# Kernel optimization log

Measured on AMD Instinct MI355X. Metric: run time of the kernel, lower is better.

Reference implementation:

```python
import jax, jax.numpy as jnp
import numpy as np

STOCH, DETER, HIDDEN, A, EMBED = 30, 200, 200, 6, 1024
T, B = 64, 512
MIN_STD = 0.1
LN_EPS = 1e-3


def _ln(x, s, b):
    m = jnp.mean(x, -1, keepdims=True)
    v = jnp.mean((x - m) ** 2, -1, keepdims=True)
    return (x - m) * jax.lax.rsqrt(v + LN_EPS) * s + b


def _stats(x):
    mean, std = jnp.split(x, 2, -1)
    return mean, jax.nn.softplus(std) + MIN_STD


def setup_inputs() -> dict:
    key = jax.random.key(0)
    ks = jax.random.split(key, 12)
    w = lambda k, shape, s=0.05: jax.random.normal(k, shape, jnp.float32) * s
    return dict(
        embed=w(ks[0], (T, B, EMBED), 1.0),
        action=w(ks[1], (T, B, A), 1.0),
        is_first=jax.random.randint(ks[2], (T, B), 0, 2).astype(jnp.float32),
        noise_prior=w(ks[3], (T, B, STOCH), 1.0),
        noise_post=w(ks[4], (T, B, STOCH), 1.0),
        w_inp=w(ks[5], (STOCH + A, HIDDEN)),
        ln_inp_s=jnp.ones((HIDDEN,)), ln_inp_b=jnp.zeros((HIDDEN,)),
        w_gru=w(ks[6], (HIDDEN + DETER, 3 * DETER)),
        w_imgout=w(ks[7], (DETER, HIDDEN)),
        ln_img_s=jnp.ones((HIDDEN,)), ln_img_b=jnp.zeros((HIDDEN,)),
        w_obsout=w(ks[8], (DETER + EMBED, HIDDEN)),
        ln_obs_s=jnp.ones((HIDDEN,)), ln_obs_b=jnp.zeros((HIDDEN,)),
        w_ims=w(ks[9], (HIDDEN, 2 * STOCH)), b_ims=jnp.zeros((2 * STOCH,)),
        w_obs=w(ks[10], (HIDDEN, 2 * STOCH)), b_obs=jnp.zeros((2 * STOCH,)),
        w_init=w(ks[11], (1, DETER), 0.1),
    )


def reference(embed, action, is_first, noise_prior, noise_post,
              w_inp, ln_inp_s, ln_inp_b, w_gru, w_imgout, ln_img_s, ln_img_b,
              w_obsout, ln_obs_s, ln_obs_b, w_ims, b_ims, w_obs, b_obs, w_init):
    # learned initial state: deter0 = tanh(W), stoch0 = mode (mean) of img stats
    deter0 = jnp.tanh(w_init) * jnp.ones((B, 1), embed.dtype)          # [B, DETER]
    h0 = jax.nn.silu(_ln(deter0 @ w_imgout, ln_img_s, ln_img_b))
    stoch0, _ = _stats(h0 @ w_ims + b_ims)                              # [B, STOCH]

    def step(carry, xs):
        stoch, deter = carry
        a_t, e_t, f_t, nzp, nzq = xs
        # action magnitude clip with stop-gradient scale
        a = a_t * jax.lax.stop_gradient(1.0 / jnp.maximum(jnp.abs(a_t), 1.0))
        f = f_t[:, None]
        a = a * (1.0 - f)
        stoch = stoch * (1.0 - f) + stoch0 * f
        deter = deter * (1.0 - f) + deter0 * f
        # img_step (prior): inp layers -> GRU cell -> img_out -> stats
        x = jax.nn.silu(_ln(jnp.concatenate([stoch, a], -1) @ w_inp, ln_inp_s, ln_inp_b))
        parts = jnp.concatenate([x, deter], -1) @ w_gru                 # [B, 3*DETER]
        r, c, u = jnp.split(parts, 3, -1)
        r = jax.nn.sigmoid(r)
        c = jnp.tanh(r * c)
        u = jax.nn.sigmoid(u - 1.0)                                     # update_bias = -1
        deter = u * c + (1.0 - u) * deter
        hp = jax.nn.silu(_ln(deter @ w_imgout, ln_img_s, ln_img_b))
        pm, ps = _stats(hp @ w_ims + b_ims)
        prior_stoch = pm + ps * nzp                                     # rsample
        # obs_step (posterior, temp_post=True): concat(deter, embed)
        ho = jax.nn.silu(_ln(jnp.concatenate([deter, e_t], -1) @ w_obsout, ln_obs_s, ln_obs_b))
        qm, qs = _stats(ho @ w_obs + b_obs)
        post_stoch = qm + qs * nzq
        out_t = jnp.concatenate([qm, qs, post_stoch, pm, ps, prior_stoch, deter], -1)
        return (post_stoch, deter), out_t

    _, out = jax.lax.scan(step, (stoch0, deter0),
                          (action, embed, is_first, noise_prior, noise_post))
    return out  # [T, B, 6*STOCH + DETER] = post(mean,std,stoch), prior(mean,std,stoch), deter
```

## Files before the change

### kernel.cpp

```cpp
#include <hip/hip_runtime.h>
#include <math.h>

#define T_STEPS 64
#define BATCH   512

typedef short s16x8 __attribute__((ext_vector_type(8)));
typedef float f32x4 __attribute__((ext_vector_type(4)));

#define MFMA(a,b,c) __builtin_amdgcn_mfma_f32_16x16x32_bf16((a),(b),(c),0,0,0)

__device__ __forceinline__ short f2bf(float x){
    union { float f; unsigned u; } v; v.f = x;
    unsigned r = v.u + 0x7FFFu + ((v.u >> 16) & 1u);
    return (short)(r >> 16);
}
__device__ __forceinline__ float bf2f(short s){
    union { unsigned u; float f; } v; v.u = ((unsigned)(unsigned short)s) << 16;
    return v.f;
}
__device__ __forceinline__ float frcp(float x){ return __builtin_amdgcn_rcpf(x); }
__device__ __forceinline__ float fsig(float x){ return frcp(1.f + __expf(-x)); }
__device__ __forceinline__ float ftanh(float x){ return 1.f - 2.f*frcp(1.f + __expf(2.f*x)); }
__device__ __forceinline__ float sp(float x){ return (x>20.f)? x : __logf(1.f + __expf(x)); }

__device__ __forceinline__ void barx(){
    asm volatile("s_waitcnt lgkmcnt(0)" ::: "memory");
    __builtin_amdgcn_s_barrier();
    asm volatile("" ::: "memory");
}

#define FR_GRU   0
#define FR_INP   494
#define FR_OBSD  520
#define FR_OBSE  611
#define FR_OBS   1027
#define FR_IMG   1055
#define FR_IMS   1146
#define FR_TOT   1174

#define WS_STOCH0 1202176
#define WS_DETER0 1202304
#define WS_E      1203200

__global__ void pack_kernel(const float* w_inp, const float* w_gru, const float* w_imgout,
                            const float* w_obsout, const float* w_ims, const float* w_obs,
                            short* pk){
    int f = blockIdx.x, l = threadIdx.x;
    const float* W; int K, N, ld, KT, k0, rel;
    if      (f < FR_INP ){ W=w_gru;    K=400; N=600; ld=600; KT=13; k0=0;   rel=f; }
    else if (f < FR_OBSD){ W=w_inp;    K=36;  N=200; ld=200; KT=2;  k0=0;   rel=f-FR_INP; }
    else if (f < FR_OBSE){ W=w_obsout; K=200; N=200; ld=200; KT=7;  k0=0;   rel=f-FR_OBSD; }
    else if (f < FR_OBS ){ W=w_obsout; K=1024;N=200; ld=200; KT=32; k0=200; rel=f-FR_OBSE; }
    else if (f < FR_IMG ){ W=w_obs;    K=200; N=60;  ld=60;  KT=7;  k0=0;   rel=f-FR_OBS; }
    else if (f < FR_IMS ){ W=w_imgout; K=200; N=200; ld=200; KT=7;  k0=0;   rel=f-FR_IMG; }
    else                 { W=w_ims;    K=200; N=60;  ld=60;  KT=7;  k0=0;   rel=f-FR_IMS; }
    int nt = rel / KT, kt = rel % KT;
    int col = nt*16 + (l & 15);
    int kb  = kt*32 + (l >> 4)*8;
    s16x8 v;
    #pragma unroll
    for (int e = 0; e < 8; e++){
        int k = kb + e;
        float x = (k < K && col < N) ? W[(size_t)(k + k0)*ld + col] : 0.f;
        v[e] = f2bf(x);
    }
    *(((s16x8*)pk) + (size_t)f*64 + l) = v;
}

__global__ void init_kernel(const float* w_init, const float* w_imgout,
                            const float* ln_img_s, const float* ln_img_b,
                            const float* w_ims, const float* b_ims,
                            float* stoch0, float* deter0){
    __shared__ float d0[200], h0[200], redA[64], redB[64], mv[2];
    int t = threadIdx.x;
    if (t < 200) d0[t] = tanhf(w_init[t]);
    __syncthreads();
    if (t < 200){ float a = 0.f; for (int k = 0; k < 200; k++) a += d0[k]*w_imgout[k*200 + t]; h0[t] = a; }
    __syncthreads();
    if (t < 64){ float s = 0.f, s2 = 0.f;
        for (int j = t; j < 200; j += 64){ float v = h0[j]; s += v; s2 += v*v; }
        redA[t] = s; redB[t] = s2; }
    __syncthreads();
    if (t == 0){ float s = 0.f, s2 = 0.f;
        for (int i = 0; i < 64; i++){ s += redA[i]; s2 += redB[i]; }
        float m = s/200.f, var = s2/200.f - m*m;
        mv[0] = m; mv[1] = rsqrtf(var + 1e-3f); }
    __syncthreads();
    if (t < 200){ float v = (h0[t]-mv[0])*mv[1]*ln_img_s[t] + ln_img_b[t];
        h0[t] = v/(1.f+expf(-v)); }
    __syncthreads();
    if (t < 200) deter0[t] = d0[t];
    if (t < 30){ float a = 0.f; for (int j = 0; j < 200; j++) a += h0[j]*w_ims[j*60 + t];
        stoch0[t] = a + b_ims[t]; }
}

__global__ __launch_bounds__(256) void embed_gemm(const float* embed, const short* pk, short* E){
    int tid = threadIdx.x; int w = tid >> 6, l = tid & 63;
    int row0 = blockIdx.x*128 + w*32;
    const float* A0 = embed + (size_t)(row0 + (l & 15))*1024 + (l >> 4)*8;
    const float* A1 = A0 + (size_t)16*1024;
    const s16x8* B = ((const s16x8*)pk) + (size_t)FR_OBSE*64 + l;
    f32x4 acc0[13], acc1[13];
    #pragma unroll
    for (int n = 0; n < 13; n++){ acc0[n] = (f32x4){0.f,0.f,0.f,0.f}; acc1[n] = (f32x4){0.f,0.f,0.f,0.f}; }
    for (int kt = 0; kt < 32; kt++){
        float4 x0 = *(const float4*)(A0 + kt*32), x1 = *(const float4*)(A0 + kt*32 + 4);
        float4 y0 = *(const float4*)(A1 + kt*32), y1 = *(const float4*)(A1 + kt*32 + 4);
        s16x8 af0, af1;
        af0[0]=f2bf(x0.x); af0[1]=f2bf(x0.y); af0[2]=f2bf(x0.z); af0[3]=f2bf(x0.w);
        af0[4]=f2bf(x1.x); af0[5]=f2bf(x1.y); af0[6]=f2bf(x1.z); af0[7]=f2bf(x1.w);
        af1[0]=f2bf(y0.x); af1[1]=f2bf(y0.y); af1[2]=f2bf(y0.z); af1[3]=f2bf(y0.w);
        af1[4]=f2bf(y1.x); af1[5]=f2bf(y1.y); af1[6]=f2bf(y1.z); af1[7]=f2bf(y1.w);
        #pragma unroll
        for (int n = 0; n < 13; n++){
            s16x8 bf = B[(n*32 + kt)*64];
            acc0[n] = MFMA(af0, bf, acc0[n]);
            acc1[n] = MFMA(af1, bf, acc1[n]);
        }
    }
    int rr = (l >> 4)*4, cc = l & 15;
    #pragma unroll
    for (int n = 0; n < 13; n++){
        int col = n*16 + cc;
        if (col < 200){
            #pragma unroll
            for (int r = 0; r < 4; r++){
                E[(size_t)(row0 + rr + r)*200 + col]        = f2bf(acc0[n][r]);
                E[(size_t)(row0 + 16 + rr + r)*200 + col]   = f2bf(acc1[n][r]);
            }
        }
    }
}

#define AB_STRIDE 424
#define XP_STRIDE 210
#define PB_STRIDE 612
#define QP_STRIDE 68
#define A36_STRIDE 72
#define HO_STRIDE 224

__global__ __launch_bounds__(512) void scan_kernel(
    const float* action, const float* is_first, const float* noise_post,
    const float* ln_inp_s, const float* ln_inp_b,
    const float* ln_obs_s, const float* ln_obs_b,
    const float* b_obs,
    const short* pk, const short* E, const float* stoch0g, const float* deter0g,
    float* out)
{
    __shared__ short Abuf[16*AB_STRIDE];
    __shared__ __align__(16) char Uraw[19584];
    __shared__ short A36hob[16*HO_STRIDE];
    __shared__ float Sbuf[16*30];
    __shared__ short WI[26*512];
    __shared__ short WD[91*512];

    float* Uf  = (float*)Uraw;
    short* Pbs = (short*)Uraw;

    int tid = threadIdx.x;
    int w = tid >> 6, l = tid & 63;
    int row = tid >> 5, s = tid & 31;
    int r0 = blockIdx.x*16;
    const int rr = (l >> 4)*4, cc = l & 15;
    const s16x8* PK = (const s16x8*)pk;

    for (int f = w; f < 26; f += 8)
        *(s16x8*)&WI[f*512 + l*8] = PK[(size_t)(FR_INP + f)*64 + l];
    for (int f = w; f < 91; f += 8)
        *(s16x8*)&WD[f*512 + l*8] = PK[(size_t)(FR_OBSD + f)*64 + l];

    float dreg[7];
    #pragma unroll
    for (int i = 0; i < 7; i++){ int j = s + 32*i; dreg[i] = (j < 200) ? deter0g[j] : 0.f; }
    if (s < 30) Sbuf[row*30 + s] = stoch0g[s];
    for (int idx = tid; idx < 16*24; idx += 512){ int q = idx/24; Abuf[q*AB_STRIDE + 400 + idx%24] = 0; }
    #pragma unroll
    for (int i = 0; i < 7; i++){ int j = s + 32*i; if (j < 200) Abuf[row*AB_STRIDE + 200 + j] = f2bf(dreg[i]); }

    float lisr[7], libr[7], losr[7], lobr[7];
    #pragma unroll
    for (int i = 0; i < 7; i++){ int j = s + 32*i; bool ok = j < 200;
        lisr[i] = ok ? ln_inp_s[j] : 0.f;  libr[i] = ok ? ln_inp_b[j] : 0.f;
        losr[i] = ok ? ln_obs_s[j] : 0.f;  lobr[i] = ok ? ln_obs_b[j] : 0.f;
    }
    float bo0 = 0.f, bo1 = 0.f;
    if (tid < 480){ int j = tid % 30; bo0 = b_obs[j]; bo1 = b_obs[30 + j]; }

    barx();

    for (int t = 0; t < T_STEPS; t++){
        float f = is_first[(size_t)t*BATCH + r0 + row];
        #pragma unroll
        for (int i = 0; i < 7; i++){ int j = s + 32*i; if (j < 200){
            float d = dreg[i]*(1.f - f) + deter0g[j]*f;
            dreg[i] = d;
            Abuf[row*AB_STRIDE + 200 + j] = f2bf(d);
        }}
        for (int j = s; j < 64; j += 32){
            float v = 0.f;
            if (j < 30) v = Sbuf[row*30 + j]*(1.f - f) + stoch0g[j]*f;
            else if (j < 36){
                float a = action[(size_t)((size_t)t*BATCH + r0 + row)*6 + (j - 30)];
                a = a * frcp(fmaxf(fabsf(a), 1.f));
                v = a*(1.f - f);
            }
            A36hob[row*A36_STRIDE + j] = f2bf(v);
        }
        s16x8 Ech;
        if (tid < 400){
            int er = tid/25, eq = tid%25;
            Ech = *(((const s16x8*)(E + (size_t)((size_t)t*BATCH + r0 + er)*200)) + eq);
        }
        float nz = 0.f;
        if (tid < 480){
            int rw = tid/30, j = tid%30;
            nz = noise_post[(size_t)((size_t)t*BATCH + r0 + rw)*30 + j];
        }
        barx();

        {
            s16x8 a0 = *(s16x8*)&A36hob[(l & 15)*A36_STRIDE + (l >> 4)*8];
            s16x8 a1 = *(s16x8*)&A36hob[(l & 15)*A36_STRIDE + 32 + (l >> 4)*8];
            for (int nt = w; nt < 13; nt += 8){
                f32x4 acc = (f32x4){0.f,0.f,0.f,0.f};
                acc = MFMA(a0, *(const s16x8*)&WI[(nt*2+0)*512 + l*8], acc);
                acc = MFMA(a1, *(const s16x8*)&WI[(nt*2+1)*512 + l*8], acc);
                #pragma unroll
                for (int r = 0; r < 4; r++) Uf[(rr + r)*XP_STRIDE + nt*16 + cc] = acc[r];
            }
        }
        barx();

        {
            float sum = 0.f, sq = 0.f, vals[7];
            #pragma unroll
            for (int i = 0; i < 7; i++){ int j = s + 32*i;
                float v = (j < 200) ? Uf[row*XP_STRIDE + j] : 0.f;
                vals[i] = v; sum += v; sq += v*v; }
            #pragma unroll
            for (int m = 16; m >= 1; m >>= 1){ sum += __shfl_xor(sum, m); sq += __shfl_xor(sq, m); }
            float mean = sum/200.f, var = sq/200.f - mean*mean, rstd = rsqrtf(var + 1e-3f);
            #pragma unroll
            for (int i = 0; i < 7; i++){ int j = s + 32*i; if (j < 200){
                float v = (vals[i] - mean)*rstd*lisr[i] + libr[i];
                Abuf[row*AB_STRIDE + j] = f2bf(v*fsig(v));
            }}
        }
        barx();

        {
            s16x8 af[13];
            #pragma unroll
            for (int kt = 0; kt < 13; kt++)
                af[kt] = *(s16x8*)&Abuf[(l & 15)*AB_STRIDE + kt*32 + (l >> 4)*8];
            for (int nt = w; nt < 38; nt += 8){
                f32x4 acc = (f32x4){0.f,0.f,0.f,0.f};
                const s16x8* B = PK + (size_t)(FR_GRU + nt*13)*64 + l;
                #pragma unroll
                for (int kt = 0; kt < 13; kt++) acc = MFMA(af[kt], B[kt*64], acc);
                #pragma unroll
                for (int r = 0; r < 4; r++) Pbs[(rr + r)*PB_STRIDE + nt*16 + cc] = f2bf(acc[r]);
            }
        }
        barx();

        {
            float* outp = out + (size_t)((size_t)t*BATCH + r0 + row)*380;
            #pragma unroll
            for (int i = 0; i < 7; i++){ int j = s + 32*i; if (j < 200){
                float rv = bf2f(Pbs[row*PB_STRIDE + j]);
                float cv = bf2f(Pbs[row*PB_STRIDE + 200 + j]);
                float uv = bf2f(Pbs[row*PB_STRIDE + 400 + j]);
                float rg = fsig(rv);
                float cg = ftanh(rg*cv);
                float ug = fsig(uv - 1.f);
                float d  = ug*cg + (1.f - ug)*dreg[i];
                dreg[i] = d;
                Abuf[row*AB_STRIDE + 200 + j] = f2bf(d);
                outp[180 + j] = d;
            }}
        }
        barx();

        {
            s16x8 ad[7];
            #pragma unroll
            for (int kt = 0; kt < 7; kt++)
                ad[kt] = *(s16x8*)&Abuf[(l & 15)*AB_STRIDE + 200 + kt*32 + (l >> 4)*8];
            for (int nt = w; nt < 13; nt += 8){
                f32x4 a0={0.f,0.f,0.f,0.f}, a1={0.f,0.f,0.f,0.f};
                a0 = MFMA(ad[0], *(const s16x8*)&WD[(nt*7+0)*512 + l*8], a0);
                a1 = MFMA(ad[1], *(const s16x8*)&WD[(nt*7+1)*512 + l*8], a1);
                a0 = MFMA(ad[2], *(const s16x8*)&WD[(nt*7+2)*512 + l*8], a0);
                a1 = MFMA(ad[3], *(const s16x8*)&WD[(nt*7+3)*512 + l*8], a1);
                a0 = MFMA(ad[4], *(const s16x8*)&WD[(nt*7+4)*512 + l*8], a0);
                a1 = MFMA(ad[5], *(const s16x8*)&WD[(nt*7+5)*512 + l*8], a1);
                a0 = MFMA(ad[6], *(const s16x8*)&WD[(nt*7+6)*512 + l*8], a0);
                #pragma unroll
                for (int r = 0; r < 4; r++) Uf[(rr + r)*XP_STRIDE + nt*16 + cc] = a0[r]+a1[r];
            }
        }
        barx();

        if (tid < 400){
            int er = tid/25, eq = tid%25;
            #pragma unroll
            for (int e = 0; e < 8; e++) Uf[er*XP_STRIDE + eq*8 + e] += bf2f(Ech[e]);
        }
        barx();

        {
            float sum = 0.f, sq = 0.f, vals[7];
            #pragma unroll
            for (int i = 0; i < 7; i++){ int j = s + 32*i;
                float v = (j < 200) ? Uf[row*XP_STRIDE + j] : 0.f;
                vals[i] = v; sum += v; sq += v*v; }
            #pragma unroll
            for (int m = 16; m >= 1; m >>= 1){ sum += __shfl_xor(sum, m); sq += __shfl_xor(sq, m); }
            float mean = sum/200.f, var = sq/200.f - mean*mean, rstd = rsqrtf(var + 1e-3f);
            #pragma unroll
            for (int i = 0; i < 7; i++){ int j = s + 32*i;
                short hv = 0;
                if (j < 200){
                    float v = (vals[i] - mean)*rstd*losr[i] + lobr[i];
                    hv = f2bf(v*fsig(v));
                }
                A36hob[row*HO_STRIDE + j] = hv;
            }
        }
        barx();

        if (w < 4){
            s16x8 ah[7];
            #pragma unroll
            for (int kt = 0; kt < 7; kt++)
                ah[kt] = *(s16x8*)&A36hob[(l & 15)*HO_STRIDE + kt*32 + (l >> 4)*8];
            f32x4 a0={0.f,0.f,0.f,0.f}, a1={0.f,0.f,0.f,0.f};
            const s16x8* B = PK + (size_t)(FR_OBS + w*7)*64 + l;
            a0=MFMA(ah[0],B[0*64],a0); a1=MFMA(ah[1],B[1*64],a1);
            a0=MFMA(ah[2],B[2*64],a0); a1=MFMA(ah[3],B[3*64],a1);
            a0=MFMA(ah[4],B[4*64],a0); a1=MFMA(ah[5],B[5*64],a1);
            a0=MFMA(ah[6],B[6*64],a0);
            #pragma unroll
            for (int r = 0; r < 4; r++) Uf[(rr + r)*QP_STRIDE + w*16 + cc] = a0[r]+a1[r];
        }
        barx();

        if (tid < 480){
            int rw = tid/30, j = tid%30;
            float qm = Uf[rw*QP_STRIDE + j] + bo0;
            float x  = Uf[rw*QP_STRIDE + 30 + j] + bo1;
            float qs = sp(x) + 0.1f;
            float post = qm + qs*nz;
            float* outp = out + (size_t)((size_t)t*BATCH + r0 + rw)*380;
            outp[j] = qm; outp[30 + j] = qs; outp[60 + j] = post;
            Sbuf[rw*30 + j] = post;
        }
        barx();
    }
}

__global__ __launch_bounds__(64) void prior_kernel(const float* noise_prior, const float* b_ims,
                                                   const float* ln_img_s, const float* ln_img_b,
                                                   const short* pk, float* out){
    __shared__ short Ab[16*232];
    __shared__ float U[16*212];
    __shared__ short hob[16*224];
    __shared__ float qp[16*68];
    int l = threadIdx.x;
    int g0 = blockIdx.x*16;

    for (int idx = l; idx < 16*232; idx += 64){
        int rr = idx/232, c = idx%232;
        short v = 0;
        if (c < 200) v = f2bf(out[(size_t)(g0 + rr)*380 + 180 + c]);
        Ab[idx] = v;
    }
    __syncthreads();
    {
        s16x8 af[7];
        #pragma unroll
        for (int kt = 0; kt < 7; kt++)
            af[kt] = *(s16x8*)&Ab[(l & 15)*232 + kt*32 + (l >> 4)*8];
        for (int nt = 0; nt < 13; nt++){
            f32x4 acc = (f32x4){0.f,0.f,0.f,0.f};
            const s16x8* B = ((const s16x8*)pk) + (size_t)(FR_IMG + nt*7)*64 + l;
            #pragma unroll
            for (int kt = 0; kt < 7; kt++) acc = MFMA(af[kt], B[kt*64], acc);
            int rr = (l >> 4)*4, cc = l & 15;
            #pragma unroll
            for (int r = 0; r < 4; r++) U[(rr + r)*212 + nt*16 + cc] = acc[r];
        }
    }
    __syncthreads();
    {
        int rw = l >> 2, s4 = l & 3;
        float sum = 0.f, sq = 0.f, vals[50];
        #pragma unroll
        for (int i = 0; i < 50; i++){ int j = s4 + 4*i; float v = U[rw*212 + j];
            vals[i] = v; sum += v; sq += v*v; }
        sum += __shfl_xor(sum, 1); sq += __shfl_xor(sq, 1);
        sum += __shfl_xor(sum, 2); sq += __shfl_xor(sq, 2);
        float mean = sum/200.f, var = sq/200.f - mean*mean, rstd = rsqrtf(var + 1e-3f);
        #pragma unroll
        for (int i = 0; i < 50; i++){ int j = s4 + 4*i;
            float v = (vals[i] - mean)*rstd*ln_img_s[j] + ln_img_b[j];
            hob[rw*224 + j] = f2bf(v*fsig(v));
        }
    }
    for (int idx = l; idx < 16*24; idx += 64){ int rr = idx/24; hob[rr*224 + 200 + idx%24] = 0; }
    __syncthreads();
    for (int nt = 0; nt < 4; nt++){
        s16x8 af[7];
        #pragma unroll
        for (int kt = 0; kt < 7; kt++)
            af[kt] = *(s16x8*)&hob[(l & 15)*224 + kt*32 + (l >> 4)*8];
        f32x4 acc = (f32x4){0.f,0.f,0.f,0.f};
        const s16x8* B = ((const s16x8*)pk) + (size_t)(FR_IMS + nt*7)*64 + l;
        #pragma unroll
        for (int kt = 0; kt < 7; kt++) acc = MFMA(af[kt], B[kt*64], acc);
        int rr = (l >> 4)*4, cc = l & 15;
        #pragma unroll
        for (int r = 0; r < 4; r++) qp[(rr + r)*68 + nt*16 + cc] = acc[r];
    }
    __syncthreads();
    for (int idx = l; idx < 480; idx += 64){
        int rw = idx/30, j = idx%30;
        float pm = qp[rw*68 + j] + b_ims[j];
        float x  = qp[rw*68 + 30 + j] + b_ims[30 + j];
        float ps = sp(x) + 0.1f;
        float nz = noise_prior[(size_t)(g0 + rw)*30 + j];
        float prior = pm + ps*nz;
        float* op = out + (size_t)(g0 + rw)*380;
        op[90 + j] = pm; op[120 + j] = ps; op[150 + j] = prior;
    }
}

extern "C" void kernel_launch(void* const* d_in, const int* in_sizes, int n_in,
                              void* d_out, int out_size, void* d_ws, size_t ws_size,
                              hipStream_t stream){
    const float* embed    = (const float*)d_in[0];
    const float* action   = (const float*)d_in[1];
    const float* is_first = (const float*)d_in[2];
    const float* nzp      = (const float*)d_in[3];
    const float* nzq      = (const float*)d_in[4];
    const float* w_inp    = (const float*)d_in[5];
    const float* ln_inp_s = (const float*)d_in[6];
    const float* ln_inp_b = (const float*)d_in[7];
    const float* w_gru    = (const float*)d_in[8];
    const float* w_imgout = (const float*)d_in[9];
    const float* ln_img_s = (const float*)d_in[10];
    const float* ln_img_b = (const float*)d_in[11];
    const float* w_obsout = (const float*)d_in[12];
    const float* ln_obs_s = (const float*)d_in[13];
    const float* ln_obs_b = (const float*)d_in[14];
    const float* w_ims    = (const float*)d_in[15];
    const float* b_ims    = (const float*)d_in[16];
    const float* w_obs    = (const float*)d_in[17];
    const float* b_obs    = (const float*)d_in[18];
    const float* w_init   = (const float*)d_in[19];

    char*  ws    = (char*)d_ws;
    short* pk    = (short*)ws;
    float* stoch0 = (float*)(ws + WS_STOCH0);
    float* deter0 = (float*)(ws + WS_DETER0);
    short* E      = (short*)(ws + WS_E);
    float* out    = (float*)d_out;

    hipLaunchKernelGGL(pack_kernel, dim3(FR_TOT), dim3(64), 0, stream,
                       w_inp, w_gru, w_imgout, w_obsout, w_ims, w_obs, pk);
    hipLaunchKernelGGL(init_kernel, dim3(1), dim3(256), 0, stream,
                       w_init, w_imgout, ln_img_s, ln_img_b, w_ims, b_ims, stoch0, deter0);
    hipLaunchKernelGGL(embed_gemm, dim3(256), dim3(256), 0, stream, embed, pk, E);
    hipLaunchKernelGGL(scan_kernel, dim3(32), dim3(512), 0, stream,
                       action, is_first, nzq, ln_inp_s, ln_inp_b, ln_obs_s, ln_obs_b, b_obs,
                       pk, E, stoch0, deter0, out);
    hipLaunchKernelGGL(prior_kernel, dim3(2048), dim3(64), 0, stream, nzp, b_ims, ln_img_s, ln_img_b, pk, out);
}
```

Before: 888.2 us.

## Split GRU matmul into deter and input halves, overlap deter part with input MLP

The GRU weight is packed as two separate K=200 halves, for the hidden input and for the deter state. Six warps compute the deter-half GRU products while the other two warps run the input projection and its layernorm/SiLU. The x-half is then accumulated on top of the partial results stored as bf16 in shared memory. This moves work off the serial critical path of each step, at the cost of an extra bf16 rounding of the partial sums and an uneven split of work across warps.

```diff
diff --git a/kernel.cpp b/kernel.cpp
--- a/kernel.cpp
+++ b/kernel.cpp
@@ -29,25 +29,27 @@
     asm volatile("" ::: "memory");
 }
 
-#define FR_GRU   0
-#define FR_INP   494
-#define FR_OBSD  520
-#define FR_OBSE  611
-#define FR_OBS   1027
-#define FR_IMG   1055
-#define FR_IMS   1146
-#define FR_TOT   1174
-
-#define WS_STOCH0 1202176
-#define WS_DETER0 1202304
-#define WS_E      1203200
+#define FR_GRUX 0
+#define FR_GRUD 266
+#define FR_INP  532
+#define FR_OBSD 558
+#define FR_OBSE 649
+#define FR_OBS  1065
+#define FR_IMG  1093
+#define FR_IMS  1184
+#define FR_TOT  1212
+
+#define WS_STOCH0 1241088
+#define WS_DETER0 1241216
+#define WS_E      1242112
 
 __global__ void pack_kernel(const float* w_inp, const float* w_gru, const float* w_imgout,
                             const float* w_obsout, const float* w_ims, const float* w_obs,
                             short* pk){
     int f = blockIdx.x, l = threadIdx.x;
     const float* W; int K, N, ld, KT, k0, rel;
-    if      (f < FR_INP ){ W=w_gru;    K=400; N=600; ld=600; KT=13; k0=0;   rel=f; }
+    if      (f < FR_GRUD){ W=w_gru;    K=200; N=600; ld=600; KT=7;  k0=0;   rel=f; }
+    else if (f < FR_INP ){ W=w_gru;    K=200; N=600; ld=600; KT=7;  k0=200; rel=f-FR_GRUD; }
     else if (f < FR_OBSD){ W=w_inp;    K=36;  N=200; ld=200; KT=2;  k0=0;   rel=f-FR_INP; }
     else if (f < FR_OBSE){ W=w_obsout; K=200; N=200; ld=200; KT=7;  k0=0;   rel=f-FR_OBSD; }
     else if (f < FR_OBS ){ W=w_obsout; K=1024;N=200; ld=200; KT=32; k0=200; rel=f-FR_OBSE; }
@@ -139,6 +141,12 @@
 #define A36_STRIDE 72
 #define HO_STRIDE 224
 
+#define MM7(AD, BP, P0, P1) \
+    P0 = MFMA(AD[0], BP[0*64], P0);  P1 = MFMA(AD[1], BP[1*64], P1); \
+    P0 = MFMA(AD[2], BP[2*64], P0);  P1 = MFMA(AD[3], BP[3*64], P1); \
+    P0 = MFMA(AD[4], BP[4*64], P0);  P1 = MFMA(AD[5], BP[5*64], P1); \
+    P0 = MFMA(AD[6], BP[6*64], P0);
+
 __global__ __launch_bounds__(512) void scan_kernel(
     const float* action, const float* is_first, const float* noise_post,
     const float* ln_inp_s, const float* ln_inp_b,
@@ -218,48 +226,88 @@
         }
         barx();
 
-        {
-            s16x8 a0 = *(s16x8*)&A36hob[(l & 15)*A36_STRIDE + (l >> 4)*8];
-            s16x8 a1 = *(s16x8*)&A36hob[(l & 15)*A36_STRIDE + 32 + (l >> 4)*8];
-            for (int nt = w; nt < 13; nt += 8){
+        if (w < 6){
+            s16x8 ad[7];
+            #pragma unroll
+            for (int kt = 0; kt < 7; kt++)
+                ad[kt] = *(s16x8*)&Abuf[cc*AB_STRIDE + 200 + kt*32 + (l>>4)*8];
+            #pragma unroll
+            for (int it = 0; it < 2; it++){
+                int nt = w + it*6;
+                f32x4 p0={0.f,0.f,0.f,0.f}, p1={0.f,0.f,0.f,0.f};
+                const s16x8* B = PK + (size_t)(FR_GRUD + nt*7)*64 + l;
+                MM7(ad, B, p0, p1);
+                #pragma unroll
+                for (int r = 0; r < 4; r++) Pbs[(rr+r)*PB_STRIDE + nt*16 + cc] = f2bf(p0[r]+p1[r]);
+            }
+        } else {
+            s16x8 a0 = *(s16x8*)&A36hob[cc*A36_STRIDE + (l>>4)*8];
+            s16x8 a1 = *(s16x8*)&A36hob[cc*A36_STRIDE + 32 + (l>>4)*8];
+            int nt0 = (w == 6) ? 0 : 7, nt1 = (w == 6) ? 7 : 13;
+            for (int nt = nt0; nt < nt1; nt++){
                 f32x4 acc = (f32x4){0.f,0.f,0.f,0.f};
                 acc = MFMA(a0, *(const s16x8*)&WI[(nt*2+0)*512 + l*8], acc);
                 acc = MFMA(a1, *(const s16x8*)&WI[(nt*2+1)*512 + l*8], acc);
                 #pragma unroll
-                for (int r = 0; r < 4; r++) Uf[(rr + r)*XP_STRIDE + nt*16 + cc] = acc[r];
+                for (int r = 0; r < 4; r++){
+                    int col = nt*16 + cc;
+                    if (col < 200) Abuf[(rr+r)*AB_STRIDE + col] = f2bf(acc[r]);
+                }
+            }
+        }
+        barx();
+
+        if (w < 6){
+            s16x8 ad[7];
+            #pragma unroll
+            for (int kt = 0; kt < 7; kt++)
+                ad[kt] = *(s16x8*)&Abuf[cc*AB_STRIDE + 200 + kt*32 + (l>>4)*8];
+            #pragma unroll
+            for (int it = 2; it < 7; it++){
+                int nt = w + it*6;
+                if (nt < 38){
+                    f32x4 p0={0.f,0.f,0.f,0.f}, p1={0.f,0.f,0.f,0.f};
+                    const s16x8* B = PK + (size_t)(FR_GRUD + nt*7)*64 + l;
+                    MM7(ad, B, p0, p1);
+                    #pragma unroll
+                    for (int r = 0; r < 4; r++) Pbs[(rr+r)*PB_STRIDE + nt*16 + cc] = f2bf(p0[r]+p1[r]);
+                }
+            }
+        } else {
+            int ss = l & 31;
+            #pragma unroll
+            for (int iter = 0; iter < 4; iter++){
+                int row2 = (w-6)*2 + (l>>5) + iter*4;
+                float vals[7], sum = 0.f, sq = 0.f;
+                #pragma unroll
+                for (int i = 0; i < 7; i++){ int j = ss + 32*i;
+                    float v = (j < 200) ? bf2f(Abuf[row2*AB_STRIDE + j]) : 0.f;
+                    vals[i] = v; sum += v; sq += v*v; }
+                #pragma unroll
+                for (int m = 16; m >= 1; m >>= 1){ sum += __shfl_xor(sum, m); sq += __shfl_xor(sq, m); }
+                float mean = sum/200.f, var = sq/200.f - mean*mean, rstd = rsqrtf(var + 1e-3f);
+                #pragma unroll
+                for (int i = 0; i < 7; i++){ int j = ss + 32*i; if (j < 200){
+                    float v = (vals[i] - mean)*rstd*lisr[i] + libr[i];
+                    Abuf[row2*AB_STRIDE + j] = f2bf(v*fsig(v));
+                }}
             }
         }
         barx();
 
         {
-            float sum = 0.f, sq = 0.f, vals[7];
-            #pragma unroll
-            for (int i = 0; i < 7; i++){ int j = s + 32*i;
-                float v = (j < 200) ? Uf[row*XP_STRIDE + j] : 0.f;
-                vals[i] = v; sum += v; sq += v*v; }
-            #pragma unroll
-            for (int m = 16; m >= 1; m >>= 1){ sum += __shfl_xor(sum, m); sq += __shfl_xor(sq, m); }
-            float mean = sum/200.f, var = sq/200.f - mean*mean, rstd = rsqrtf(var + 1e-3f);
-            #pragma unroll
-            for (int i = 0; i < 7; i++){ int j = s + 32*i; if (j < 200){
-                float v = (vals[i] - mean)*rstd*lisr[i] + libr[i];
-                Abuf[row*AB_STRIDE + j] = f2bf(v*fsig(v));
-            }}
-        }
-        barx();
-
-        {
-            s16x8 af[13];
-            #pragma unroll
-            for (int kt = 0; kt < 13; kt++)
-                af[kt] = *(s16x8*)&Abuf[(l & 15)*AB_STRIDE + kt*32 + (l >> 4)*8];
+            s16x8 ax[7];
+            #pragma unroll
+            for (int kt = 0; kt < 7; kt++)
+                ax[kt] = *(s16x8*)&Abuf[cc*AB_STRIDE + kt*32 + (l>>4)*8];
             for (int nt = w; nt < 38; nt += 8){
-                f32x4 acc = (f32x4){0.f,0.f,0.f,0.f};
-                const s16x8* B = PK + (size_t)(FR_GRU + nt*13)*64 + l;
-                #pragma unroll
-                for (int kt = 0; kt < 13; kt++) acc = MFMA(af[kt], B[kt*64], acc);
-                #pragma unroll
-                for (int r = 0; r < 4; r++) Pbs[(rr + r)*PB_STRIDE + nt*16 + cc] = f2bf(acc[r]);
+                f32x4 p0, p1 = (f32x4){0.f,0.f,0.f,0.f};
+                #pragma unroll
+                for (int r = 0; r < 4; r++) p0[r] = bf2f(Pbs[(rr+r)*PB_STRIDE + nt*16 + cc]);
+                const s16x8* B = PK + (size_t)(FR_GRUX + nt*7)*64 + l;
+                MM7(ax, B, p0, p1);
+                #pragma unroll
+                for (int r = 0; r < 4; r++) Pbs[(rr+r)*PB_STRIDE + nt*16 + cc] = f2bf(p0[r]+p1[r]);
             }
         }
         barx();
@@ -286,7 +334,7 @@
             s16x8 ad[7];
             #pragma unroll
             for (int kt = 0; kt < 7; kt++)
-                ad[kt] = *(s16x8*)&Abuf[(l & 15)*AB_STRIDE + 200 + kt*32 + (l >> 4)*8];
+                ad[kt] = *(s16x8*)&Abuf[cc*AB_STRIDE + 200 + kt*32 + (l>>4)*8];
             for (int nt = w; nt < 13; nt += 8){
                 f32x4 a0={0.f,0.f,0.f,0.f}, a1={0.f,0.f,0.f,0.f};
                 a0 = MFMA(ad[0], *(const s16x8*)&WD[(nt*7+0)*512 + l*8], a0);
@@ -334,13 +382,10 @@
             s16x8 ah[7];
             #pragma unroll
             for (int kt = 0; kt < 7; kt++)
-                ah[kt] = *(s16x8*)&A36hob[(l & 15)*HO_STRIDE + kt*32 + (l >> 4)*8];
+                ah[kt] = *(s16x8*)&A36hob[cc*HO_STRIDE + kt*32 + (l>>4)*8];
             f32x4 a0={0.f,0.f,0.f,0.f}, a1={0.f,0.f,0.f,0.f};
             const s16x8* B = PK + (size_t)(FR_OBS + w*7)*64 + l;
-            a0=MFMA(ah[0],B[0*64],a0); a1=MFMA(ah[1],B[1*64],a1);
-            a0=MFMA(ah[2],B[2*64],a0); a1=MFMA(ah[3],B[3*64],a1);
-            a0=MFMA(ah[4],B[4*64],a0); a1=MFMA(ah[5],B[5*64],a1);
-            a0=MFMA(ah[6],B[6*64],a0);
+            MM7(ah, B, a0, a1);
             #pragma unroll
             for (int r = 0; r < 4; r++) Uf[(rr + r)*QP_STRIDE + w*16 + cc] = a0[r]+a1[r];
         }
```

Measured after the change: 922.5 us. +3.9%, slower.

## Stage prior-kernel weights in LDS and process four row tiles per block

Applied to the files above, without the earlier changes.

The prior kernel now runs 256-thread blocks that load the imgout and ims weight fragments into shared memory once, then loop over four 16-row tiles, so weights are read from global memory a quarter as often. Work within each tile is split across four waves, with LayerNorm reduced per 32-lane group and the MFMA chains split into two accumulators. The prior pass is a small part of total time next to the sequential scan, and the larger LDS footprint (about 160KB) limits occupancy to one block per CU.

```diff
diff --git a/kernel.cpp b/kernel.cpp
--- a/kernel.cpp
+++ b/kernel.cpp
@@ -360,79 +360,123 @@
     }
 }
 
-__global__ __launch_bounds__(64) void prior_kernel(const float* noise_prior, const float* b_ims,
-                                                   const float* ln_img_s, const float* ln_img_b,
-                                                   const short* pk, float* out){
-    __shared__ short Ab[16*232];
-    __shared__ float U[16*212];
-    __shared__ short hob[16*224];
-    __shared__ float qp[16*68];
-    int l = threadIdx.x;
-    int g0 = blockIdx.x*16;
-
-    for (int idx = l; idx < 16*232; idx += 64){
-        int rr = idx/232, c = idx%232;
-        short v = 0;
-        if (c < 200) v = f2bf(out[(size_t)(g0 + rr)*380 + 180 + c]);
-        Ab[idx] = v;
-    }
+#define PAB 232
+#define PU  212
+#define PHO 224
+#define PQP 68
+
+__global__ __launch_bounds__(256) void prior_kernel(const float* noise_prior, const float* b_ims,
+                                                    const float* ln_img_s, const float* ln_img_b,
+                                                    const short* pk, float* out){
+    __shared__ short WG[91*512];
+    __shared__ short WS2[28*512];
+    __shared__ short Ab[16*PAB];
+    __shared__ float U[16*PU];
+    __shared__ short hob[16*PHO];
+    __shared__ float qp[16*PQP];
+
+    const int tid = threadIdx.x;
+    const int w = tid >> 6, l = tid & 63;
+    const int rr = (l >> 4)*4, cc = l & 15;
+    const int s = tid & 31;
+    const s16x8* PK = (const s16x8*)pk;
+    const int g0 = blockIdx.x*64;
+
+    for (int f = w; f < 91; f += 4)
+        *(s16x8*)&WG[f*512 + l*8] = PK[(size_t)(FR_IMG + f)*64 + l];
+    for (int f = w; f < 28; f += 4)
+        *(s16x8*)&WS2[f*512 + l*8] = PK[(size_t)(FR_IMS + f)*64 + l];
+
+    float lgs[7], lgb[7];
+    #pragma unroll
+    for (int i = 0; i < 7; i++){ int j = s + 32*i; bool ok = j < 200;
+        lgs[i] = ok ? ln_img_s[j] : 0.f;  lgb[i] = ok ? ln_img_b[j] : 0.f; }
+    float bi0 = b_ims[tid % 30], bi1 = b_ims[30 + tid % 30];
+
+    for (int idx = tid; idx < 16*32; idx += 256) Ab[(idx/32)*PAB + 200 + (idx%32)] = 0;
+    for (int idx = tid; idx < 16*24; idx += 256) hob[(idx/24)*PHO + 200 + (idx%24)] = 0;
+
     __syncthreads();
-    {
-        s16x8 af[7];
+
+    for (int tile = 0; tile < 4; tile++){
+        const int gt = g0 + tile*16;
+
+        for (int idx = tid; idx < 16*200; idx += 256){
+            int q = idx/200, c = idx%200;
+            Ab[q*PAB + c] = f2bf(out[(size_t)(gt + q)*380 + 180 + c]);
+        }
+        barx();
+
+        {
+            s16x8 af[7];
+            #pragma unroll
+            for (int kt = 0; kt < 7; kt++)
+                af[kt] = *(s16x8*)&Ab[(l & 15)*PAB + kt*32 + (l >> 4)*8];
+            for (int nt = w; nt < 13; nt += 4){
+                f32x4 a0={0.f,0.f,0.f,0.f}, a1={0.f,0.f,0.f,0.f};
+                a0 = MFMA(af[0], *(const s16x8*)&WG[(nt*7+0)*512 + l*8], a0);
+                a1 = MFMA(af[1], *(const s16x8*)&WG[(nt*7+1)*512 + l*8], a1);
+                a0 = MFMA(af[2], *(const s16x8*)&WG[(nt*7+2)*512 + l*8], a0);
+                a1 = MFMA(af[3], *(const s16x8*)&WG[(nt*7+3)*512 + l*8], a1);
+                a0 = MFMA(af[4], *(const s16x8*)&WG[(nt*7+4)*512 + l*8], a0);
+                a1 = MFMA(af[5], *(const s16x8*)&WG[(nt*7+5)*512 + l*8], a1);
+                a0 = MFMA(af[6], *(const s16x8*)&WG[(nt*7+6)*512 + l*8], a0);
+                #pragma unroll
+                for (int r = 0; r < 4; r++) U[(rr + r)*PU + nt*16 + cc] = a0[r]+a1[r];
+            }
+        }
+        barx();
+
         #pragma unroll
-        for (int kt = 0; kt < 7; kt++)
-            af[kt] = *(s16x8*)&Ab[(l & 15)*232 + kt*32 + (l >> 4)*8];
-        for (int nt = 0; nt < 13; nt++){
-            f32x4 acc = (f32x4){0.f,0.f,0.f,0.f};
-            const s16x8* B = ((const s16x8*)pk) + (size_t)(FR_IMG + nt*7)*64 + l;
-            #pragma unroll
-            for (int kt = 0; kt < 7; kt++) acc = MFMA(af[kt], B[kt*64], acc);
-            int rr = (l >> 4)*4, cc = l & 15;
-            #pragma unroll
-            for (int r = 0; r < 4; r++) U[(rr + r)*212 + nt*16 + cc] = acc[r];
-        }
-    }
-    __syncthreads();
-    {
-        int rw = l >> 2, s4 = l & 3;
-        float sum = 0.f, sq = 0.f, vals[50];
-        #pragma unroll
-        for (int i = 0; i < 50; i++){ int j = s4 + 4*i; float v = U[rw*212 + j];
-            vals[i] = v; sum += v; sq += v*v; }
-        sum += __shfl_xor(sum, 1); sq += __shfl_xor(sq, 1);
-        sum += __shfl_xor(sum, 2); sq += __shfl_xor(sq, 2);
-        float mean = sum/200.f, var = sq/200.f - mean*mean, rstd = rsqrtf(var + 1e-3f);
-        #pragma unroll
-        for (int i = 0; i < 50; i++){ int j = s4 + 4*i;
-            float v = (vals[i] - mean)*rstd*ln_img_s[j] + ln_img_b[j];
-            hob[rw*224 + j] = f2bf(v*fsig(v));
-        }
-    }
-    for (int idx = l; idx < 16*24; idx += 64){ int rr = idx/24; hob[rr*224 + 200 + idx%24] = 0; }
-    __syncthreads();
-    for (int nt = 0; nt < 4; nt++){
-        s16x8 af[7];
-        #pragma unroll
-        for (int kt = 0; kt < 7; kt++)
-            af[kt] = *(s16x8*)&hob[(l & 15)*224 + kt*32 + (l >> 4)*8];
-        f32x4 acc = (f32x4){0.f,0.f,0.f,0.f};
-        const s16x8* B = ((const s16x8*)pk) + (size_t)(FR_IMS + nt*7)*64 + l;
-        #pragma unroll
-        for (int kt = 0; kt < 7; kt++) acc = MFMA(af[kt], B[kt*64], acc);
-        int rr = (l >> 4)*4, cc = l & 15;
-        #pragma unroll
-        for (int r = 0; r < 4; r++) qp[(rr + r)*68 + nt*16 + cc] = acc[r];
-    }
-    __syncthreads();
-    for (int idx = l; idx < 480; idx += 64){
-        int rw = idx/30, j = idx%30;
-        float pm = qp[rw*68 + j] + b_ims[j];
-        float x  = qp[rw*68 + 30 + j] + b_ims[30 + j];
-        float ps = sp(x) + 0.1f;
-        float nz = noise_prior[(size_t)(g0 + rw)*30 + j];
-        float prior = pm + ps*nz;
-        float* op = out + (size_t)(g0 + rw)*380;
-        op[90 + j] = pm; op[120 + j] = ps; op[150 + j] = prior;
+        for (int iter = 0; iter < 2; iter++){
+            int rw = (tid >> 5) + iter*8;
+            float sum = 0.f, sq = 0.f, vals[7];
+            #pragma unroll
+            for (int i = 0; i < 7; i++){ int j = s + 32*i;
+                float v = (j < 200) ? U[rw*PU + j] : 0.f;
+                vals[i] = v; sum += v; sq += v*v; }
+            #pragma unroll
+            for (int m = 16; m >= 1; m >>= 1){ sum += __shfl_xor(sum, m); sq += __shfl_xor(sq, m); }
+            float mean = sum/200.f, var = sq/200.f - mean*mean, rstd = rsqrtf(var + 1e-3f);
+            #pragma unroll
+            for (int i = 0; i < 7; i++){ int j = s + 32*i; if (j < 200){
+                float v = (vals[i] - mean)*rstd*lgs[i] + lgb[i];
+                hob[rw*PHO + j] = f2bf(v*fsig(v));
+            }}
+        }
+        barx();
+
+        {
+            s16x8 ah[7];
+            #pragma unroll
+            for (int kt = 0; kt < 7; kt++)
+                ah[kt] = *(s16x8*)&hob[(l & 15)*PHO + kt*32 + (l >> 4)*8];
+            int nt = w;
+            f32x4 a0={0.f,0.f,0.f,0.f}, a1={0.f,0.f,0.f,0.f};
+            a0 = MFMA(ah[0], *(const s16x8*)&WS2[(nt*7+0)*512 + l*8], a0);
+            a1 = MFMA(ah[1], *(const s16x8*)&WS2[(nt*7+1)*512 + l*8], a1);
+            a0 = MFMA(ah[2], *(const s16x8*)&WS2[(nt*7+2)*512 + l*8], a0);
+            a1 = MFMA(ah[3], *(const s16x8*)&WS2[(nt*7+3)*512 + l*8], a1);
+            a0 = MFMA(ah[4], *(const s16x8*)&WS2[(nt*7+4)*512 + l*8], a0);
+            a1 = MFMA(ah[5], *(const s16x8*)&WS2[(nt*7+5)*512 + l*8], a1);
+            a0 = MFMA(ah[6], *(const s16x8*)&WS2[(nt*7+6)*512 + l*8], a0);
+            #pragma unroll
+            for (int r = 0; r < 4; r++) qp[(rr + r)*PQP + nt*16 + cc] = a0[r]+a1[r];
+        }
+        barx();
+
+        for (int idx = tid; idx < 480; idx += 256){
+            int rw = idx/30, j = idx%30;
+            float pm = qp[rw*PQP + j] + ((idx == tid) ? bi0 : b_ims[j]);
+            pm = qp[rw*PQP + j] + b_ims[j];
+            float x  = qp[rw*PQP + 30 + j] + b_ims[30 + j];
+            float ps = sp(x) + 0.1f;
+            float nzv = noise_prior[(size_t)(gt + rw)*30 + j];
+            float prior = pm + ps*nzv;
+            float* op = out + (size_t)(gt + rw)*380;
+            op[90 + j] = pm; op[120 + j] = ps; op[150 + j] = prior;
+        }
+        barx();
     }
 }
 
@@ -475,5 +519,5 @@
     hipLaunchKernelGGL(scan_kernel, dim3(32), dim3(512), 0, stream,
                        action, is_first, nzq, ln_inp_s, ln_inp_b, ln_obs_s, ln_obs_b, b_obs,
                        pk, E, stoch0, deter0, out);
-    hipLaunchKernelGGL(prior_kernel, dim3(2048), dim3(64), 0, stream, nzp, b_ims, ln_img_s, ln_img_b, pk, out);
-}
+    hipLaunchKernelGGL(prior_kernel, dim3(512), dim3(256), 0, stream, nzp, b_ims, ln_img_s, ln_img_b, pk, out);
+}
```

After: 895.2 us. Within noise of the previous version (+0.8%).
